# Optimization experiments

Measured on AMD Instinct MI355X. Metric: run time of the kernel, lower is better.

Reference implementation:

```python
import jax, jax.numpy as jnp
import numpy as np

N, E, D_IN, HD, H = 50000, 800000, 768, 64, 4
HC = HD * H


def _gat(x, src, dst, etypes, lin_w, att_src, att_dst, edge_emb, lin_edge_w, att_edge,
         bias, res_w, res_b, ln_g, ln_b):
    # Faithful PyG GATConv (edge_dim, concat=True, add_self_loops=True with
    # fill_value='mean', negative_slope=0.2) + residual + LayerNorm. Eval mode: no dropout.
    n = x.shape[0]
    h, c = att_src.shape
    xs = (x @ lin_w).reshape(n, h, c)                      # [N,H,C]
    a_src = jnp.einsum('nhc,hc->nh', xs, att_src)          # [N,H]
    a_dst = jnp.einsum('nhc,hc->nh', xs, att_dst)
    eattr = edge_emb[etypes]                               # [E,ed]
    ones = jnp.ones((etypes.shape[0],), x.dtype)
    cnt = jax.ops.segment_sum(ones, dst, num_segments=n)
    # self-loop edge_attr = mean of incoming edge attrs per node (fill_value='mean')
    loop_attr = jax.ops.segment_sum(eattr, dst, num_segments=n) / jnp.maximum(cnt, 1.0)[:, None]
    loop = jnp.arange(n, dtype=src.dtype)
    src_a = jnp.concatenate([src, loop])
    dst_a = jnp.concatenate([dst, loop])
    e_all = jnp.concatenate([eattr, loop_attr], 0)
    a_edge = jnp.einsum('ehc,hc->eh', (e_all @ lin_edge_w).reshape(-1, h, c), att_edge)
    alpha = jax.nn.leaky_relu(a_src[src_a] + a_dst[dst_a] + a_edge, 0.2)   # [Ea,H]
    # edge softmax over incoming edges of each destination node
    amax = jax.ops.segment_max(alpha, dst_a, num_segments=n)
    ea = jnp.exp(alpha - amax[dst_a])
    denom = jax.ops.segment_sum(ea, dst_a, num_segments=n)
    w = ea / (denom[dst_a] + 1e-16)
    out = jax.ops.segment_sum(xs[src_a] * w[:, :, None], dst_a, num_segments=n)
    out = out.reshape(n, h * c) + bias + (x @ res_w + res_b)
    mu = out.mean(-1, keepdims=True)
    var = jnp.mean((out - mu) ** 2, -1, keepdims=True)
    return (out - mu) * jax.lax.rsqrt(var + 1e-5) * ln_g + ln_b


def _forward(features, positions,
             fe_w1, fe_b1, fe_w2, fe_b2, fe_pos_w, fe_pos_b, fe_type_emb, fe_out_w, fe_out_b,
             g1_lin_w, g1_att_src, g1_att_dst, g1_edge_emb, g1_lin_edge_w, g1_att_edge,
             g1_bias, g1_res_w, g1_res_b, g1_ln_g, g1_ln_b,
             g2_lin_w, g2_att_src, g2_att_dst, g2_edge_emb, g2_lin_edge_w, g2_att_edge,
             g2_bias, g2_res_w, g2_res_b, g2_ln_g, g2_ln_b,
             cls_w, cls_b,
             edge_index, aspect_indices, edge_types, node_types):
    # EnhancedFeatureExtractor (eval: dropout = identity)
    hfe = jax.nn.relu(features @ fe_w1 + fe_b1) @ fe_w2 + fe_b2
    hfe = hfe + fe_type_emb[node_types] + positions[:, None] @ fe_pos_w + fe_pos_b
    hfe = hfe @ fe_out_w + fe_out_b
    src, dst = edge_index[0], edge_index[1]
    hid = _gat(hfe, src, dst, edge_types, g1_lin_w, g1_att_src, g1_att_dst, g1_edge_emb,
               g1_lin_edge_w, g1_att_edge, g1_bias, g1_res_w, g1_res_b, g1_ln_g, g1_ln_b)
    hid = jax.nn.relu(hid)
    hid = _gat(hid, src, dst, edge_types, g2_lin_w, g2_att_src, g2_att_dst, g2_edge_emb,
               g2_lin_edge_w, g2_att_edge, g2_bias, g2_res_w, g2_res_b, g2_ln_g, g2_ln_b)
    return hid[aspect_indices] @ cls_w + cls_b


def setup_inputs() -> dict:
    key = jax.random.key(0)
    ks = jax.random.split(key, 40)
    d = {}
    d['features'] = jax.random.normal(ks[0], (N, D_IN), jnp.float32)
    d['edge_index'] = jax.random.randint(ks[1], (2, E), 0, N, jnp.int32)
    d['aspect_indices'] = jax.random.randint(ks[2], (4096,), 0, N, jnp.int32)
    d['edge_types'] = jax.random.randint(ks[3], (E,), 0, 4, jnp.int32)
    d['node_types'] = jax.random.randint(ks[4], (N,), 0, 3, jnp.int32)
    d['positions'] = jax.random.uniform(ks[5], (N,), jnp.float32)

    def rn(i, shape, s=0.05):
        return s * jax.random.normal(ks[i], shape, jnp.float32)

    d['fe_w1'] = rn(6, (D_IN, HD)); d['fe_b1'] = rn(7, (HD,))
    d['fe_w2'] = rn(8, (HD, HD));   d['fe_b2'] = rn(9, (HD,))
    d['fe_pos_w'] = rn(10, (1, HD)); d['fe_pos_b'] = rn(11, (HD,))
    d['fe_type_emb'] = rn(12, (3, HD))
    d['fe_out_w'] = rn(13, (HD, HD)); d['fe_out_b'] = rn(14, (HD,))
    d['g1_lin_w'] = rn(15, (HD, HC))
    d['g1_att_src'] = rn(16, (H, HD)); d['g1_att_dst'] = rn(17, (H, HD))
    d['g1_edge_emb'] = rn(18, (4, 4)); d['g1_lin_edge_w'] = rn(19, (4, HC))
    d['g1_att_edge'] = rn(20, (H, HD))
    d['g1_bias'] = rn(21, (HC,)); d['g1_res_w'] = rn(22, (HD, HC)); d['g1_res_b'] = rn(23, (HC,))
    d['g1_ln_g'] = jnp.ones((HC,), jnp.float32); d['g1_ln_b'] = jnp.zeros((HC,), jnp.float32)
    d['g2_lin_w'] = rn(24, (HC, HD))
    d['g2_att_src'] = rn(25, (1, HD)); d['g2_att_dst'] = rn(26, (1, HD))
    d['g2_edge_emb'] = rn(27, (4, 4)); d['g2_lin_edge_w'] = rn(28, (4, HD))
    d['g2_att_edge'] = rn(29, (1, HD))
    d['g2_bias'] = rn(30, (HD,)); d['g2_res_w'] = rn(31, (HC, HD)); d['g2_res_b'] = rn(32, (HD,))
    d['g2_ln_g'] = jnp.ones((HD,), jnp.float32); d['g2_ln_b'] = jnp.zeros((HD,), jnp.float32)
    d['cls_w'] = rn(33, (HD, 3)); d['cls_b'] = rn(34, (3,))
    return d


def reference(features, edge_index, aspect_indices, edge_types, node_types, positions,
              fe_w1, fe_b1, fe_w2, fe_b2, fe_pos_w, fe_pos_b, fe_type_emb, fe_out_w, fe_out_b,
              g1_lin_w, g1_att_src, g1_att_dst, g1_edge_emb, g1_lin_edge_w, g1_att_edge,
              g1_bias, g1_res_w, g1_res_b, g1_ln_g, g1_ln_b,
              g2_lin_w, g2_att_src, g2_att_dst, g2_edge_emb, g2_lin_edge_w, g2_att_edge,
              g2_bias, g2_res_w, g2_res_b, g2_ln_g, g2_ln_b,
              cls_w, cls_b):
    return _forward(features, positions,
                    fe_w1, fe_b1, fe_w2, fe_b2, fe_pos_w, fe_pos_b, fe_type_emb, fe_out_w, fe_out_b,
                    g1_lin_w, g1_att_src, g1_att_dst, g1_edge_emb, g1_lin_edge_w, g1_att_edge,
                    g1_bias, g1_res_w, g1_res_b, g1_ln_g, g1_ln_b,
                    g2_lin_w, g2_att_src, g2_att_dst, g2_edge_emb, g2_lin_edge_w, g2_att_edge,
                    g2_bias, g2_res_w, g2_res_b, g2_ln_g, g2_ln_b,
                    cls_w, cls_b,
                    edge_index, aspect_indices, edge_types, node_types)
```

## Files before the change

### kernel.cpp

```cpp
#include <hip/hip_runtime.h>


#define LRELU(x) ((x) > 0.f ? (x) : 0.2f * (x))

typedef __attribute__((ext_vector_type(8))) short short8;
typedef __attribute__((ext_vector_type(4))) float floatx4;

__device__ __forceinline__ unsigned short f2bf(float x) {
    union { float f; unsigned int u; } v; v.f = x;
    unsigned int r = (v.u + 0x7FFFu + ((v.u >> 16) & 1u)) >> 16;
    return (unsigned short)r;
}
__device__ __forceinline__ unsigned int pkbf(float lo, float hi) {
    unsigned int a = __float_as_uint(lo) + 0x8000u;
    unsigned int b = __float_as_uint(hi) + 0x8000u;
    return __builtin_amdgcn_perm(b, a, 0x07060302u);
}
__device__ __forceinline__ float bflo(unsigned int u) {
    return __uint_as_float(u << 16);
}
__device__ __forceinline__ float bfhi(unsigned int u) {
    return __uint_as_float(u & 0xFFFF0000u);
}
__device__ __forceinline__ float bf1(unsigned short u) {
    return __uint_as_float(((unsigned int)u) << 16);
}

__global__ __launch_bounds__(64) void k_tables(
    const float* __restrict__ e_emb1, const float* __restrict__ lew1,
    const float* __restrict__ ae1,
    const float* __restrict__ e_emb2, const float* __restrict__ lew2,
    const float* __restrict__ ae2,
    float* __restrict__ aet1, float* __restrict__ aet2)
{
    __shared__ float M1[16];
    __shared__ float M2[4];
    int t = threadIdx.x;
    if (t < 16) {
        int d = t >> 2, h = t & 3;
        float s = 0.f;
        for (int c = 0; c < 64; ++c) s += lew1[d * 256 + h * 64 + c] * ae1[h * 64 + c];
        M1[d * 4 + h] = s;
    }
    if (t < 4) {
        float s = 0.f;
        for (int c = 0; c < 64; ++c) s += lew2[t * 64 + c] * ae2[c];
        M2[t] = s;
    }
    __syncthreads();
    if (t < 16) {
        int ty = t >> 2, h = t & 3;
        float s = 0.f;
        for (int d = 0; d < 4; ++d) s += e_emb1[ty * 4 + d] * M1[d * 4 + h];
        aet1[ty * 4 + h] = s;
    }
    if (t < 4) {
        float s = 0.f;
        for (int d = 0; d < 4; ++d) s += e_emb2[t * 4 + d] * M2[d];
        aet2[t] = s;
    }
}

__global__ __launch_bounds__(256) void k_bswz_fe1(
    const float* __restrict__ w1, unsigned short* __restrict__ out)
{
    for (int idx = blockIdx.x * 256 + threadIdx.x; idx < 768 * 64;
         idx += gridDim.x * 256) {
        int k = idx >> 6, col = idx & 63;
        int c = k >> 6, kl = k & 63, kg = kl >> 3, j = kl & 7;
        out[((c * 8 + kg) * 64 + col) * 8 + j] = f2bf(w1[k * 64 + col]);
    }
}

template<int K, int NH>
__global__ __launch_bounds__(256) void k_bswz2(
    const float* __restrict__ B1, const float* __restrict__ B2,
    unsigned short* __restrict__ out)
{
    const int NC = 2 * NH;
    for (int idx = blockIdx.x * 256 + threadIdx.x; idx < K * NC;
         idx += gridDim.x * 256) {
        int k = idx / NC, col = idx % NC;
        float v = (col < NH) ? B1[k * NH + col] : B2[k * NH + col - NH];
        int c = k >> 6, kl = k & 63, kg = kl >> 3, j = kl & 7;
        int ct = col >> 7, cl = col & 127;
        out[(((c * (NC / 128) + ct) * 8 + kg) * 128 + cl) * 8 + j] = f2bf(v);
    }
}

__global__ __launch_bounds__(256) void k_fe1(
    const float* __restrict__ feat, const unsigned short* __restrict__ bswz,
    const float* __restrict__ b1, float* __restrict__ t1, int N)
{
    __shared__ __align__(16) unsigned short A_lds[8 * 64 * 8];
    int t = threadIdx.x;
    int wv = t >> 6, lane = t & 63;
    int quad = lane >> 4, l16 = lane & 15;
    long n0 = (long)blockIdx.x * 64;

    floatx4 acc[4];
#pragma unroll
    for (int i = 0; i < 4; ++i) acc[i] = (floatx4){0.f, 0.f, 0.f, 0.f};

    int srow = t >> 2, sf4 = t & 3;
    long arow = n0 + srow;
    if (arow >= N) arow = N - 1;
    const float* fbase = feat + arow * 768 + sf4 * 16;
    int col = wv * 16 + l16;

    for (int kc = 0; kc < 768; kc += 64) {
        __syncthreads();
        float4 v0 = *(const float4*)(fbase + kc);
        float4 v1 = *(const float4*)(fbase + kc + 4);
        float4 v2 = *(const float4*)(fbase + kc + 8);
        float4 v3 = *(const float4*)(fbase + kc + 12);
        uint4 w0 = {pkbf(v0.x, v0.y), pkbf(v0.z, v0.w),
                    pkbf(v1.x, v1.y), pkbf(v1.z, v1.w)};
        uint4 w1p = {pkbf(v2.x, v2.y), pkbf(v2.z, v2.w),
                     pkbf(v3.x, v3.y), pkbf(v3.z, v3.w)};
        *(uint4*)&A_lds[((2 * sf4) * 64 + srow) * 8] = w0;
        *(uint4*)&A_lds[((2 * sf4 + 1) * 64 + srow) * 8] = w1p;
        __syncthreads();
        int ci = kc >> 6;
#pragma unroll
        for (int s = 0; s < 2; ++s) {
            int kg0 = s * 4 + quad;
            short8 bfrag = *(const short8*)&bswz[((ci * 8 + kg0) * 64 + col) * 8];
#pragma unroll
            for (int mt = 0; mt < 4; ++mt) {
                short8 afrag = *(const short8*)&A_lds[(kg0 * 64 + mt * 16 + l16) * 8];
                acc[mt] = __builtin_amdgcn_mfma_f32_16x16x32_bf16(
                    afrag, bfrag, acc[mt], 0, 0, 0);
            }
        }
    }
    float bb = b1[col];
#pragma unroll
    for (int mt = 0; mt < 4; ++mt) {
#pragma unroll
        for (int r = 0; r < 4; ++r) {
            long m = n0 + mt * 16 + quad * 4 + r;
            if (m < N) t1[m * 64 + col] = fmaxf(acc[mt][r] + bb, 0.f);
        }
    }
}

__global__ __launch_bounds__(256) void k_fe2(
    const float* __restrict__ t1, const float* __restrict__ w2,
    const float* __restrict__ b2, const int* __restrict__ ntypes,
    const float* __restrict__ temb, const float* __restrict__ pos,
    const float* __restrict__ posw, const float* __restrict__ posb,
    const float* __restrict__ outw, const float* __restrict__ outb,
    float* __restrict__ hfe)
{
    __shared__ float l1[256];
    __shared__ float l2[256];
    int t = threadIdx.x;
    long base = (long)blockIdx.x * 256;
    l1[t] = t1[base + t];
    __syncthreads();
    int r = t >> 6, c = t & 63;
    float acc = 0.f;
#pragma unroll 8
    for (int k = 0; k < 64; ++k) acc += l1[r * 64 + k] * w2[k * 64 + c];
    long n = (long)blockIdx.x * 4 + r;
    int nt = ntypes[n];
    acc += b2[c] + temb[nt * 64 + c] + pos[n] * posw[c] + posb[c];
    l2[r * 64 + c] = acc;
    __syncthreads();
    float acc2 = 0.f;
#pragma unroll 8
    for (int k = 0; k < 64; ++k) acc2 += l2[r * 64 + k] * outw[k * 64 + c];
    hfe[n * 64 + c] = acc2 + outb[c];
}

template<int K, int NH>
__global__ __launch_bounds__(256) void k_prep_gemm(
    const float* __restrict__ A, const unsigned short* __restrict__ bswz,
    const float* __restrict__ bias, const float* __restrict__ res_b,
    unsigned short* __restrict__ xsb, float* __restrict__ resp, int N)
{
    constexpr int CT = (2 * NH) / 128;
    __shared__ __align__(16) unsigned short A_lds[8 * 64 * 8];
    int t = threadIdx.x;
    int wv = t >> 6, lane = t & 63;
    int quad = lane >> 4, l16 = lane & 15;
    long n0 = (long)blockIdx.x * 64;
    int by = blockIdx.y;

    floatx4 acc[4][2];
#pragma unroll
    for (int i = 0; i < 4; ++i)
#pragma unroll
        for (int j = 0; j < 2; ++j) acc[i][j] = (floatx4){0.f, 0.f, 0.f, 0.f};

    int srow = t >> 2, sf4 = t & 3;
    long arow = n0 + srow;
    if (arow >= N) arow = N - 1;
    const float* abase = A + arow * (long)K + sf4 * 16;

    for (int kc = 0; kc < K; kc += 64) {
        __syncthreads();
        float4 v0 = *(const float4*)(abase + kc);
        float4 v1 = *(const float4*)(abase + kc + 4);
        float4 v2 = *(const float4*)(abase + kc + 8);
        float4 v3 = *(const float4*)(abase + kc + 12);
        uint4 w0 = {pkbf(v0.x, v0.y), pkbf(v0.z, v0.w),
                    pkbf(v1.x, v1.y), pkbf(v1.z, v1.w)};
        uint4 w1p = {pkbf(v2.x, v2.y), pkbf(v2.z, v2.w),
                     pkbf(v3.x, v3.y), pkbf(v3.z, v3.w)};
        *(uint4*)&A_lds[((2 * sf4) * 64 + srow) * 8] = w0;
        *(uint4*)&A_lds[((2 * sf4 + 1) * 64 + srow) * 8] = w1p;
        __syncthreads();
        int ci = kc >> 6;
#pragma unroll
        for (int s = 0; s < 2; ++s) {
            int kg0 = s * 4 + quad;
#pragma unroll
            for (int nt = 0; nt < 2; ++nt) {
                short8 bfrag = *(const short8*)&bswz[
                    (((ci * CT + by) * 8 + kg0) * 128 + wv * 32 + nt * 16 + l16) * 8];
#pragma unroll
                for (int mt = 0; mt < 4; ++mt) {
                    short8 afrag = *(const short8*)&A_lds[(kg0 * 64 + mt * 16 + l16) * 8];
                    acc[mt][nt] = __builtin_amdgcn_mfma_f32_16x16x32_bf16(
                        afrag, bfrag, acc[mt][nt], 0, 0, 0);
                }
            }
        }
    }
#pragma unroll
    for (int nt = 0; nt < 2; ++nt) {
        int gc = by * 128 + wv * 32 + nt * 16 + l16;
        bool isl = gc < NH;
        int oc = isl ? gc : gc - NH;
        float badd = isl ? 0.f : (bias[oc] + res_b[oc]);
#pragma unroll
        for (int mt = 0; mt < 4; ++mt) {
#pragma unroll
            for (int r = 0; r < 4; ++r) {
                long m = n0 + mt * 16 + quad * 4 + r;
                if (m < N) {
                    float val = acc[mt][nt][r];
                    if (isl) xsb[m * NH + oc] = f2bf(val);
                    else     resp[m * NH + oc] = val + badd;
                }
            }
        }
    }
}

template<int H>
__global__ __launch_bounds__(256) void k_att(
    const unsigned short* __restrict__ xsb, const float* __restrict__ att_s,
    const float* __restrict__ att_d, float* __restrict__ a_src,
    float* __restrict__ a_dst, int N)
{
    int t = threadIdx.x;
    int wv = t >> 6, lane = t & 63;
    long n = (long)blockIdx.x * 4 + wv;
    if (n >= N) return;
    if (H == 4) {
        ushort4 u = *(const ushort4*)&xsb[n * 256 + lane * 4];
        float4 as = *(const float4*)&att_s[lane * 4];
        float4 ad = *(const float4*)&att_d[lane * 4];
        float x0 = bf1(u.x), x1 = bf1(u.y), x2 = bf1(u.z), x3 = bf1(u.w);
        float p = x0 * as.x + x1 * as.y + x2 * as.z + x3 * as.w;
        float q = x0 * ad.x + x1 * ad.y + x2 * ad.z + x3 * ad.w;
#pragma unroll
        for (int k = 8; k; k >>= 1) {
            p += __shfl_xor(p, k, 64);
            q += __shfl_xor(q, k, 64);
        }
        if ((lane & 15) == 0) {
            a_src[n * 4 + (lane >> 4)] = p;
            a_dst[n * 4 + (lane >> 4)] = q;
        }
    } else {
        float x = bf1(xsb[n * 64 + lane]);
        float p = x * att_s[lane];
        float q = x * att_d[lane];
#pragma unroll
        for (int k = 32; k; k >>= 1) {
            p += __shfl_xor(p, k, 64);
            q += __shfl_xor(q, k, 64);
        }
        if (lane == 0) { a_src[n] = p; a_dst[n] = q; }
    }
}

__global__ __launch_bounds__(256) void k_count(
    const int* __restrict__ dst, const int* __restrict__ et,
    int* __restrict__ cnt_t, int E)
{
    int e = blockIdx.x * 256 + threadIdx.x;
    if (e < E) atomicAdd(&cnt_t[dst[e] * 4 + et[e]], 1);
}

__global__ __launch_bounds__(256) void k_scan1(
    const int* __restrict__ cnt_t, int* __restrict__ row_off,
    int* __restrict__ blk_sums, int N)
{
    __shared__ int s[256];
    int t = threadIdx.x;
    int i = blockIdx.x * 256 + t;
    int v = 0;
    if (i < N) v = cnt_t[4 * i] + cnt_t[4 * i + 1] + cnt_t[4 * i + 2] + cnt_t[4 * i + 3];
    s[t] = v;
    __syncthreads();
    for (int off = 1; off < 256; off <<= 1) {
        int x = 0;
        if (t >= off) x = s[t - off];
        __syncthreads();
        s[t] += x;
        __syncthreads();
    }
    if (i < N) row_off[i] = s[t] - v;
    if (t == 255) blk_sums[blockIdx.x] = s[255];
}

__global__ __launch_bounds__(256) void k_scan2(int* __restrict__ blk_sums, int nb)
{
    __shared__ int s[256];
    int t = threadIdx.x;
    int v = (t < nb) ? blk_sums[t] : 0;
    s[t] = v;
    __syncthreads();
    for (int off = 1; off < 256; off <<= 1) {
        int x = 0;
        if (t >= off) x = s[t - off];
        __syncthreads();
        s[t] += x;
        __syncthreads();
    }
    if (t < nb) blk_sums[t] = s[t] - v;
}

__global__ __launch_bounds__(256) void k_scan3(
    int* __restrict__ row_off, int* __restrict__ cursor,
    const int* __restrict__ blk_sums, int N, int E)
{
    int t = threadIdx.x;
    int i = blockIdx.x * 256 + t;
    if (i < N) {
        int o = row_off[i] + blk_sums[blockIdx.x];
        row_off[i] = o;
        cursor[i] = o;
    }
    if (i == 0) row_off[N] = E;
}

__global__ __launch_bounds__(256) void k_scatter(
    const int* __restrict__ src, const int* __restrict__ dst,
    const int* __restrict__ et, int* __restrict__ cursor,
    int* __restrict__ csr_pack, int E)
{
    int e = blockIdx.x * 256 + threadIdx.x;
    if (e < E) {
        int d = dst[e];
        int pos = atomicAdd(&cursor[d], 1);
        csr_pack[pos] = src[e] | (et[e] << 28);
    }
}

__global__ __launch_bounds__(128) void k_gat1(
    const unsigned short* __restrict__ xs1b, const float* __restrict__ a_src,
    const float* __restrict__ a_dst, const int* __restrict__ row_off,
    const int* __restrict__ csr_pack,
    const int* __restrict__ cnt_t, const float* __restrict__ aet1,
    const float* __restrict__ ln_g, const float* __restrict__ ln_b,
    float* io)
{
    __shared__ __align__(16) float4 ws[2][64];
    __shared__ float2 aetp[2][4];
    __shared__ float red[4];
    int n = blockIdx.x;
    int t = threadIdx.x;
    int w = t >> 6, c = t & 63;
    int h0 = 2 * w;
    if (t < 8) {
        int w2 = t >> 2, ty = t & 3;
        aetp[w2][ty] = make_float2(aet1[ty * 4 + 2 * w2], aet1[ty * 4 + 2 * w2 + 1]);
    }
    int off = row_off[n], deg = row_off[n + 1] - off;
    float2 a_d = *(const float2*)&a_dst[n * 4 + h0];
    __syncthreads();
    float ael0 = 0.f, ael1 = 0.f;
    int degc = 0;
#pragma unroll
    for (int ty = 0; ty < 4; ++ty) {
        int ct = cnt_t[n * 4 + ty];
        degc += ct;
        float2 ae = aetp[w][ty];
        ael0 += (float)ct * ae.x;
        ael1 += (float)ct * ae.y;
    }
    float inv = (degc > 0) ? 1.f / (float)degc : 1.f;
    float2 a_s_self = *(const float2*)&a_src[n * 4 + h0];
    float al0 = a_s_self.x + a_d.x + ael0 * inv;
    float al1 = a_s_self.y + a_d.y + ael1 * inv;
    al0 = LRELU(al0); al1 = LRELU(al1);
    float wself0 = expf(al0), wself1 = expf(al1);
    int col = w * 128 + 2 * c;
    unsigned int uself = *(const unsigned int*)&xs1b[(long)n * 256 + col];
    float wself_l = (c < 32) ? wself0 : wself1;
    float acc0 = wself_l * bflo(uself);
    float acc1 = wself_l * bfhi(uself);
    float dp0 = 0.f, dp1 = 0.f;
    const unsigned short* xcol = xs1b + col;
    for (int base = 0; base < deg; base += 64) {
        int cnt = min(64, deg - base);
        float w0 = 0.f, w1 = 0.f;
        int s = 0;
        if (c < cnt) {
            int pk = csr_pack[off + base + c];
            s = pk & 0x0FFFFFFF;
            int ty = ((unsigned)pk) >> 28;
            float2 as2 = *(const float2*)&a_src[s * 4 + h0];
            float2 ae = aetp[w][ty];
            float a0 = as2.x + a_d.x + ae.x;
            float a1 = as2.y + a_d.y + ae.y;
            a0 = LRELU(a0); a1 = LRELU(a1);
            w0 = expf(a0); w1 = expf(a1);
        }
        dp0 += w0; dp1 += w1;
        ws[w][c] = make_float4(w0, w1, __int_as_float(s), 0.f);
        int cr = (cnt + 7) & ~7;
        for (int i = 0; i < cr; i += 8) {
#pragma unroll
            for (int u = 0; u < 8; ++u) {
                float4 p = ws[w][i + u];
                unsigned int uu = *(const unsigned int*)&xcol[
                    (long)__float_as_int(p.z) * 256];
                float wl = (c < 32) ? p.x : p.y;
                acc0 += wl * bflo(uu);
                acc1 += wl * bfhi(uu);
            }
        }
    }
#pragma unroll
    for (int k = 32; k; k >>= 1) {
        dp0 += __shfl_xor(dp0, k, 64);
        dp1 += __shfl_xor(dp1, k, 64);
    }
    float dsum = ((c < 32) ? dp0 + wself0 : dp1 + wself1) + 1e-16f;
    float2 res = *(const float2*)&io[(long)n * 256 + col];
    float v0 = acc0 / dsum + res.x;
    float v1 = acc1 / dsum + res.y;
    float s1 = v0 + v1, s2 = v0 * v0 + v1 * v1;
#pragma unroll
    for (int k = 32; k; k >>= 1) {
        s1 += __shfl_xor(s1, k, 64);
        s2 += __shfl_xor(s2, k, 64);
    }
    if (c == 0) { red[w] = s1; red[2 + w] = s2; }
    __syncthreads();
    float mu = (red[0] + red[1]) * (1.f / 256.f);
    float var = (red[2] + red[3]) * (1.f / 256.f) - mu * mu;
    float rs = rsqrtf(var + 1e-5f);
    float2 g = *(const float2*)&ln_g[col];
    float2 bln = *(const float2*)&ln_b[col];
    float y0 = fmaxf((v0 - mu) * rs * g.x + bln.x, 0.f);
    float y1 = fmaxf((v1 - mu) * rs * g.y + bln.y, 0.f);
    *(float2*)&io[(long)n * 256 + col] = make_float2(y0, y1);
}

__global__ __launch_bounds__(64) void k_gat2(
    const unsigned short* __restrict__ xs2b, const float* __restrict__ a_src,
    const float* __restrict__ a_dst, const int* __restrict__ row_off,
    const int* __restrict__ csr_pack,
    const int* __restrict__ cnt_t, const float* __restrict__ aet2,
    const float* __restrict__ ln_g, const float* __restrict__ ln_b,
    float* io)
{
    __shared__ __align__(8) float2 ws[64];
    __shared__ float aetl[4];
    int n = blockIdx.x;
    int c = threadIdx.x;
    if (c < 4) aetl[c] = aet2[c];
    int off = row_off[n], deg = row_off[n + 1] - off;
    float a_d = a_dst[n];
    float ael = 0.f;
    int degc = 0;
#pragma unroll
    for (int ty = 0; ty < 4; ++ty) {
        int ct = cnt_t[n * 4 + ty];
        degc += ct;
        ael += (float)ct * aet2[ty];
    }
    ael *= (degc > 0 ? 1.f / (float)degc : 1.f);
    float al = a_src[n] + a_d + ael;
    al = LRELU(al);
    float wself = expf(al);
    float acc = wself * bf1(xs2b[(long)n * 64 + c]);
    float dp = 0.f;
    const unsigned short* xcol = xs2b + c;
    for (int base = 0; base < deg; base += 64) {
        int cnt = min(64, deg - base);
        float we = 0.f;
        int s = 0;
        if (c < cnt) {
            int pk = csr_pack[off + base + c];
            s = pk & 0x0FFFFFFF;
            int ty = ((unsigned)pk) >> 28;
            float a = a_src[s] + a_d + aetl[ty];
            a = LRELU(a);
            we = expf(a);
        }
        dp += we;
        ws[c] = make_float2(we, __int_as_float(s));
        int cr = (cnt + 7) & ~7;
        for (int i = 0; i < cr; i += 8) {
#pragma unroll
            for (int u = 0; u < 8; ++u) {
                float2 p = ws[i + u];
                acc += p.x * bf1(xcol[(long)__float_as_int(p.y) * 64]);
            }
        }
    }
#pragma unroll
    for (int k = 32; k; k >>= 1) dp += __shfl_xor(dp, k, 64);
    float dsum = dp + wself + 1e-16f;
    float v = acc / dsum + io[(long)n * 64 + c];
    float s1 = v, s2 = v * v;
#pragma unroll
    for (int k = 32; k; k >>= 1) {
        s1 += __shfl_xor(s1, k, 64);
        s2 += __shfl_xor(s2, k, 64);
    }
    float mu = s1 * (1.f / 64.f);
    float var = s2 * (1.f / 64.f) - mu * mu;
    io[(long)n * 64 + c] = (v - mu) * rsqrtf(var + 1e-5f) * ln_g[c] + ln_b[c];
}

__global__ __launch_bounds__(256) void k_cls(
    const float* __restrict__ hid2, const int* __restrict__ asp,
    const float* __restrict__ w, const float* __restrict__ b,
    float* __restrict__ out)
{
    int g = blockIdx.x * 256 + threadIdx.x;
    int i = g / 3, j = g - i * 3;
    int a = asp[i];
    float acc = b[j];
#pragma unroll 8
    for (int cc = 0; cc < 64; ++cc) acc += hid2[(long)a * 64 + cc] * w[cc * 3 + j];
    out[i * 3 + j] = acc;
}

extern "C" void kernel_launch(void* const* d_in, const int* in_sizes, int n_in,
                              void* d_out, int out_size, void* d_ws, size_t ws_size,
                              hipStream_t stream)
{
    const float* features    = (const float*)d_in[0];
    const int*   edge_index  = (const int*)d_in[1];
    const int*   aspect      = (const int*)d_in[2];
    const int*   etypes      = (const int*)d_in[3];
    const int*   ntypes      = (const int*)d_in[4];
    const float* pos         = (const float*)d_in[5];
    const float* fe_w1       = (const float*)d_in[6];
    const float* fe_b1       = (const float*)d_in[7];
    const float* fe_w2       = (const float*)d_in[8];
    const float* fe_b2       = (const float*)d_in[9];
    const float* fe_pos_w    = (const float*)d_in[10];
    const float* fe_pos_b    = (const float*)d_in[11];
    const float* fe_type_emb = (const float*)d_in[12];
    const float* fe_out_w    = (const float*)d_in[13];
    const float* fe_out_b    = (const float*)d_in[14];
    const float* g1_lin_w    = (const float*)d_in[15];
    const float* g1_att_src  = (const float*)d_in[16];
    const float* g1_att_dst  = (const float*)d_in[17];
    const float* g1_edge_emb = (const float*)d_in[18];
    const float* g1_lin_edge = (const float*)d_in[19];
    const float* g1_att_edge = (const float*)d_in[20];
    const float* g1_bias     = (const float*)d_in[21];
    const float* g1_res_w    = (const float*)d_in[22];
    const float* g1_res_b    = (const float*)d_in[23];
    const float* g1_ln_g     = (const float*)d_in[24];
    const float* g1_ln_b     = (const float*)d_in[25];
    const float* g2_lin_w    = (const float*)d_in[26];
    const float* g2_att_src  = (const float*)d_in[27];
    const float* g2_att_dst  = (const float*)d_in[28];
    const float* g2_edge_emb = (const float*)d_in[29];
    const float* g2_lin_edge = (const float*)d_in[30];
    const float* g2_att_edge = (const float*)d_in[31];
    const float* g2_bias     = (const float*)d_in[32];
    const float* g2_res_w    = (const float*)d_in[33];
    const float* g2_res_b    = (const float*)d_in[34];
    const float* g2_ln_g     = (const float*)d_in[35];
    const float* g2_ln_b     = (const float*)d_in[36];
    const float* cls_w       = (const float*)d_in[37];
    const float* cls_b       = (const float*)d_in[38];

    const int N = in_sizes[0] / 768;
    const int E = in_sizes[1] / 2;
    const int* src = edge_index;
    const int* dst = edge_index + E;

    char* wsb = (char*)d_ws;
    size_t off = 0;
    auto alloc = [&](size_t bytes) -> char* {
        char* p = wsb + off;
        off += (bytes + 255) & ~(size_t)255;
        return p;
    };
    float* t1      = (float*)alloc((size_t)N * 64 * 4);
    float* hfe     = (float*)alloc((size_t)N * 64 * 4);
    unsigned short* xs1b = (unsigned short*)alloc((size_t)N * 256 * 2);
    unsigned short* xs2b = (unsigned short*)alloc((size_t)N * 64 * 2);
    float* rp1     = (float*)alloc((size_t)N * 256 * 4);
    float* rp2     = (float*)alloc((size_t)N * 64 * 4);
    float* a_src1  = (float*)alloc((size_t)N * 4 * 4);
    float* a_dst1  = (float*)alloc((size_t)N * 4 * 4);
    float* a_src2  = (float*)alloc((size_t)N * 4);
    float* a_dst2  = (float*)alloc((size_t)N * 4);
    int*   cnt_t   = (int*)alloc((size_t)N * 4 * 4);
    int*   row_off = (int*)alloc((size_t)(N + 1) * 4);
    int*   cursor  = (int*)alloc((size_t)N * 4);
    int*   blk     = (int*)alloc(1024);
    int*   csr_pack= (int*)alloc((size_t)E * 4);
    float* aet1    = (float*)alloc(64);
    float* aet2    = (float*)alloc(64);
    unsigned short* bz_fe1 = (unsigned short*)alloc(768 * 64 * 2);
    unsigned short* bz_p1  = (unsigned short*)alloc(64 * 512 * 2);
    unsigned short* bz_p2  = (unsigned short*)alloc(256 * 128 * 2);

    hipMemsetAsync(cnt_t, 0, (size_t)N * 4 * 4, stream);

    int mb = (N + 63) / 64;
    int ab = (N + 3) / 4;

    k_tables<<<1, 64, 0, stream>>>(g1_edge_emb, g1_lin_edge, g1_att_edge,
                                   g2_edge_emb, g2_lin_edge, g2_att_edge, aet1, aet2);
    k_bswz_fe1<<<48, 256, 0, stream>>>(fe_w1, bz_fe1);
    k_bswz2<64, 256><<<32, 256, 0, stream>>>(g1_lin_w, g1_res_w, bz_p1);
    k_bswz2<256, 64><<<32, 256, 0, stream>>>(g2_lin_w, g2_res_w, bz_p2);
    k_fe1<<<mb, 256, 0, stream>>>(features, bz_fe1, fe_b1, t1, N);
    k_fe2<<<N / 4, 256, 0, stream>>>(t1, fe_w2, fe_b2, ntypes, fe_type_emb, pos,
                                     fe_pos_w, fe_pos_b, fe_out_w, fe_out_b, hfe);
    k_prep_gemm<64, 256><<<dim3(mb, 4), 256, 0, stream>>>(
        hfe, bz_p1, g1_bias, g1_res_b, xs1b, rp1, N);
    k_att<4><<<ab, 256, 0, stream>>>(xs1b, g1_att_src, g1_att_dst, a_src1, a_dst1, N);
    int eblk = (E + 255) / 256;
    int nb = (N + 255) / 256;
    k_count<<<eblk, 256, 0, stream>>>(dst, etypes, cnt_t, E);
    k_scan1<<<nb, 256, 0, stream>>>(cnt_t, row_off, blk, N);
    k_scan2<<<1, 256, 0, stream>>>(blk, nb);
    k_scan3<<<nb, 256, 0, stream>>>(row_off, cursor, blk, N, E);
    k_scatter<<<eblk, 256, 0, stream>>>(src, dst, etypes, cursor, csr_pack, E);
    k_gat1<<<N, 128, 0, stream>>>(xs1b, a_src1, a_dst1, row_off, csr_pack,
                                  cnt_t, aet1, g1_ln_g, g1_ln_b, rp1);
    k_prep_gemm<256, 64><<<dim3(mb, 1), 256, 0, stream>>>(
        rp1, bz_p2, g2_bias, g2_res_b, xs2b, rp2, N);
    k_att<1><<<ab, 256, 0, stream>>>(xs2b, g2_att_src, g2_att_dst, a_src2, a_dst2, N);
    k_gat2<<<N, 64, 0, stream>>>(xs2b, a_src2, a_dst2, row_off, csr_pack,
                                 cnt_t, aet2, g2_ln_g, g2_ln_b, rp2);
    k_cls<<<(out_size + 255) / 256, 256, 0, stream>>>(rp2, aspect, cls_w, cls_b,
                                                      (float*)d_out);
}
```

Before: 641.6 us.

## Register-prefetch GEMM A tiles and vectorize GAT neighbor gathers across lane groups

The two MFMA GEMM kernels now load the next K-chunk of A into registers while the current chunk is consumed, so global load latency overlaps with the MFMA work. The GAT aggregation kernels are restructured so that each lane gathers 8 (gat1) or 4 (gat2) bf16 features with one wide load, and four lane groups process different neighbors in parallel before a shuffle reduction. This replaces many narrow gathers with fewer wide ones. The cost is more registers, extra cross-lane reductions, and LayerNorm statistics that must be rescaled because each value is now replicated across four lane groups.

```diff
diff --git a/kernel.cpp b/kernel.cpp
--- a/kernel.cpp
+++ b/kernel.cpp
@@ -108,18 +108,25 @@
     const float* fbase = feat + arow * 768 + sf4 * 16;
     int col = wv * 16 + l16;
 
+    float4 v0 = *(const float4*)(fbase);
+    float4 v1 = *(const float4*)(fbase + 4);
+    float4 v2 = *(const float4*)(fbase + 8);
+    float4 v3 = *(const float4*)(fbase + 12);
+
     for (int kc = 0; kc < 768; kc += 64) {
-        __syncthreads();
-        float4 v0 = *(const float4*)(fbase + kc);
-        float4 v1 = *(const float4*)(fbase + kc + 4);
-        float4 v2 = *(const float4*)(fbase + kc + 8);
-        float4 v3 = *(const float4*)(fbase + kc + 12);
         uint4 w0 = {pkbf(v0.x, v0.y), pkbf(v0.z, v0.w),
                     pkbf(v1.x, v1.y), pkbf(v1.z, v1.w)};
         uint4 w1p = {pkbf(v2.x, v2.y), pkbf(v2.z, v2.w),
                      pkbf(v3.x, v3.y), pkbf(v3.z, v3.w)};
+        __syncthreads();
         *(uint4*)&A_lds[((2 * sf4) * 64 + srow) * 8] = w0;
         *(uint4*)&A_lds[((2 * sf4 + 1) * 64 + srow) * 8] = w1p;
+        if (kc + 64 < 768) {
+            v0 = *(const float4*)(fbase + kc + 64);
+            v1 = *(const float4*)(fbase + kc + 68);
+            v2 = *(const float4*)(fbase + kc + 72);
+            v3 = *(const float4*)(fbase + kc + 76);
+        }
         __syncthreads();
         int ci = kc >> 6;
 #pragma unroll
@@ -199,18 +206,25 @@
     if (arow >= N) arow = N - 1;
     const float* abase = A + arow * (long)K + sf4 * 16;
 
+    float4 v0 = *(const float4*)(abase);
+    float4 v1 = *(const float4*)(abase + 4);
+    float4 v2 = *(const float4*)(abase + 8);
+    float4 v3 = *(const float4*)(abase + 12);
+
     for (int kc = 0; kc < K; kc += 64) {
-        __syncthreads();
-        float4 v0 = *(const float4*)(abase + kc);
-        float4 v1 = *(const float4*)(abase + kc + 4);
-        float4 v2 = *(const float4*)(abase + kc + 8);
-        float4 v3 = *(const float4*)(abase + kc + 12);
         uint4 w0 = {pkbf(v0.x, v0.y), pkbf(v0.z, v0.w),
                     pkbf(v1.x, v1.y), pkbf(v1.z, v1.w)};
         uint4 w1p = {pkbf(v2.x, v2.y), pkbf(v2.z, v2.w),
                      pkbf(v3.x, v3.y), pkbf(v3.z, v3.w)};
+        __syncthreads();
         *(uint4*)&A_lds[((2 * sf4) * 64 + srow) * 8] = w0;
         *(uint4*)&A_lds[((2 * sf4 + 1) * 64 + srow) * 8] = w1p;
+        if (kc + 64 < K) {
+            v0 = *(const float4*)(abase + kc + 64);
+            v1 = *(const float4*)(abase + kc + 68);
+            v2 = *(const float4*)(abase + kc + 72);
+            v3 = *(const float4*)(abase + kc + 76);
+        }
         __syncthreads();
         int ci = kc >> 6;
 #pragma unroll
@@ -377,6 +391,7 @@
     int n = blockIdx.x;
     int t = threadIdx.x;
     int w = t >> 6, c = t & 63;
+    int lc = c & 15, g = c >> 4;
     int h0 = 2 * w;
     if (t < 8) {
         int w2 = t >> 2, ty = t & 3;
@@ -401,13 +416,14 @@
     float al1 = a_s_self.y + a_d.y + ael1 * inv;
     al0 = LRELU(al0); al1 = LRELU(al1);
     float wself0 = expf(al0), wself1 = expf(al1);
-    int col = w * 128 + 2 * c;
-    unsigned int uself = *(const unsigned int*)&xs1b[(long)n * 256 + col];
-    float wself_l = (c < 32) ? wself0 : wself1;
-    float acc0 = wself_l * bflo(uself);
-    float acc1 = wself_l * bfhi(uself);
+
+    int col0 = w * 128 + lc * 8;
+    const unsigned short* xrow = xs1b + col0;
+    float acc[8];
+#pragma unroll
+    for (int j = 0; j < 8; ++j) acc[j] = 0.f;
     float dp0 = 0.f, dp1 = 0.f;
-    const unsigned short* xcol = xs1b + col;
+
     for (int base = 0; base < deg; base += 64) {
         int cnt = min(64, deg - base);
         float w0 = 0.f, w1 = 0.f;
@@ -428,13 +444,14 @@
         int cr = (cnt + 7) & ~7;
         for (int i = 0; i < cr; i += 8) {
 #pragma unroll
-            for (int u = 0; u < 8; ++u) {
-                float4 p = ws[w][i + u];
-                unsigned int uu = *(const unsigned int*)&xcol[
-                    (long)__float_as_int(p.z) * 256];
-                float wl = (c < 32) ? p.x : p.y;
-                acc0 += wl * bflo(uu);
-                acc1 += wl * bfhi(uu);
+            for (int u = 0; u < 2; ++u) {
+                float4 p = ws[w][i + u * 4 + g];
+                float wl = (lc < 8) ? p.x : p.y;
+                uint4 q = *(const uint4*)&xrow[(long)__float_as_int(p.z) * 256];
+                acc[0] += wl * bflo(q.x); acc[1] += wl * bfhi(q.x);
+                acc[2] += wl * bflo(q.y); acc[3] += wl * bfhi(q.y);
+                acc[4] += wl * bflo(q.z); acc[5] += wl * bfhi(q.z);
+                acc[6] += wl * bflo(q.w); acc[7] += wl * bfhi(q.w);
             }
         }
     }
@@ -443,26 +460,56 @@
         dp0 += __shfl_xor(dp0, k, 64);
         dp1 += __shfl_xor(dp1, k, 64);
     }
-    float dsum = ((c < 32) ? dp0 + wself0 : dp1 + wself1) + 1e-16f;
-    float2 res = *(const float2*)&io[(long)n * 256 + col];
-    float v0 = acc0 / dsum + res.x;
-    float v1 = acc1 / dsum + res.y;
-    float s1 = v0 + v1, s2 = v0 * v0 + v1 * v1;
+#pragma unroll
+    for (int j = 0; j < 8; ++j) {
+        acc[j] += __shfl_xor(acc[j], 16, 64);
+        acc[j] += __shfl_xor(acc[j], 32, 64);
+    }
+    uint4 us = *(const uint4*)&xrow[(long)n * 256];
+    float wself_l = (lc < 8) ? wself0 : wself1;
+    acc[0] += wself_l * bflo(us.x); acc[1] += wself_l * bfhi(us.x);
+    acc[2] += wself_l * bflo(us.y); acc[3] += wself_l * bfhi(us.y);
+    acc[4] += wself_l * bflo(us.z); acc[5] += wself_l * bfhi(us.z);
+    acc[6] += wself_l * bflo(us.w); acc[7] += wself_l * bfhi(us.w);
+    float dsum = ((lc < 8) ? dp0 + wself0 : dp1 + wself1) + 1e-16f;
+    float rd = 1.f / dsum;
+    float4 r0 = *(const float4*)&io[(long)n * 256 + col0];
+    float4 r1 = *(const float4*)&io[(long)n * 256 + col0 + 4];
+    float v[8];
+    v[0] = acc[0] * rd + r0.x; v[1] = acc[1] * rd + r0.y;
+    v[2] = acc[2] * rd + r0.z; v[3] = acc[3] * rd + r0.w;
+    v[4] = acc[4] * rd + r1.x; v[5] = acc[5] * rd + r1.y;
+    v[6] = acc[6] * rd + r1.z; v[7] = acc[7] * rd + r1.w;
+    float s1 = 0.f, s2 = 0.f;
+#pragma unroll
+    for (int j = 0; j < 8; ++j) { s1 += v[j]; s2 += v[j] * v[j]; }
 #pragma unroll
     for (int k = 32; k; k >>= 1) {
         s1 += __shfl_xor(s1, k, 64);
         s2 += __shfl_xor(s2, k, 64);
     }
-    if (c == 0) { red[w] = s1; red[2 + w] = s2; }
+    if (c == 0) { red[w] = s1 * 0.25f; red[2 + w] = s2 * 0.25f; }
     __syncthreads();
     float mu = (red[0] + red[1]) * (1.f / 256.f);
     float var = (red[2] + red[3]) * (1.f / 256.f) - mu * mu;
     float rs = rsqrtf(var + 1e-5f);
-    float2 g = *(const float2*)&ln_g[col];
-    float2 bln = *(const float2*)&ln_b[col];
-    float y0 = fmaxf((v0 - mu) * rs * g.x + bln.x, 0.f);
-    float y1 = fmaxf((v1 - mu) * rs * g.y + bln.y, 0.f);
-    *(float2*)&io[(long)n * 256 + col] = make_float2(y0, y1);
+    float4 lg0 = *(const float4*)&ln_g[col0];
+    float4 lg1 = *(const float4*)&ln_g[col0 + 4];
+    float4 lb0 = *(const float4*)&ln_b[col0];
+    float4 lb1 = *(const float4*)&ln_b[col0 + 4];
+    if (g == 0) {
+        float4 y0, y1;
+        y0.x = fmaxf((v[0] - mu) * rs * lg0.x + lb0.x, 0.f);
+        y0.y = fmaxf((v[1] - mu) * rs * lg0.y + lb0.y, 0.f);
+        y0.z = fmaxf((v[2] - mu) * rs * lg0.z + lb0.z, 0.f);
+        y0.w = fmaxf((v[3] - mu) * rs * lg0.w + lb0.w, 0.f);
+        y1.x = fmaxf((v[4] - mu) * rs * lg1.x + lb1.x, 0.f);
+        y1.y = fmaxf((v[5] - mu) * rs * lg1.y + lb1.y, 0.f);
+        y1.z = fmaxf((v[6] - mu) * rs * lg1.z + lb1.z, 0.f);
+        y1.w = fmaxf((v[7] - mu) * rs * lg1.w + lb1.w, 0.f);
+        *(float4*)&io[(long)n * 256 + col0] = y0;
+        *(float4*)&io[(long)n * 256 + col0 + 4] = y1;
+    }
 }
 
 __global__ __launch_bounds__(64) void k_gat2(
@@ -477,6 +524,7 @@
     __shared__ float aetl[4];
     int n = blockIdx.x;
     int c = threadIdx.x;
+    int lc = c & 15, g = c >> 4;
     if (c < 4) aetl[c] = aet2[c];
     int off = row_off[n], deg = row_off[n + 1] - off;
     float a_d = a_dst[n];
@@ -492,9 +540,11 @@
     float al = a_src[n] + a_d + ael;
     al = LRELU(al);
     float wself = expf(al);
-    float acc = wself * bf1(xs2b[(long)n * 64 + c]);
+
+    int colb = lc * 4;
+    const unsigned short* xrow = xs2b + colb;
+    float acc[4] = {0.f, 0.f, 0.f, 0.f};
     float dp = 0.f;
-    const unsigned short* xcol = xs2b + c;
     for (int base = 0; base < deg; base += 64) {
         int cnt = min(64, deg - base);
         float we = 0.f;
@@ -512,25 +562,50 @@
         int cr = (cnt + 7) & ~7;
         for (int i = 0; i < cr; i += 8) {
 #pragma unroll
-            for (int u = 0; u < 8; ++u) {
-                float2 p = ws[i + u];
-                acc += p.x * bf1(xcol[(long)__float_as_int(p.y) * 64]);
+            for (int u = 0; u < 2; ++u) {
+                float2 p = ws[i + u * 4 + g];
+                uint2 q = *(const uint2*)&xrow[(long)__float_as_int(p.y) * 64];
+                acc[0] += p.x * bflo(q.x); acc[1] += p.x * bfhi(q.x);
+                acc[2] += p.x * bflo(q.y); acc[3] += p.x * bfhi(q.y);
             }
         }
     }
 #pragma unroll
     for (int k = 32; k; k >>= 1) dp += __shfl_xor(dp, k, 64);
+#pragma unroll
+    for (int j = 0; j < 4; ++j) {
+        acc[j] += __shfl_xor(acc[j], 16, 64);
+        acc[j] += __shfl_xor(acc[j], 32, 64);
+    }
+    uint2 us = *(const uint2*)&xrow[(long)n * 64];
+    acc[0] += wself * bflo(us.x); acc[1] += wself * bfhi(us.x);
+    acc[2] += wself * bflo(us.y); acc[3] += wself * bfhi(us.y);
     float dsum = dp + wself + 1e-16f;
-    float v = acc / dsum + io[(long)n * 64 + c];
-    float s1 = v, s2 = v * v;
+    float rd = 1.f / dsum;
+    float4 r = *(const float4*)&io[(long)n * 64 + colb];
+    float v[4];
+    v[0] = acc[0] * rd + r.x; v[1] = acc[1] * rd + r.y;
+    v[2] = acc[2] * rd + r.z; v[3] = acc[3] * rd + r.w;
+    float s1 = v[0] + v[1] + v[2] + v[3];
+    float s2 = v[0] * v[0] + v[1] * v[1] + v[2] * v[2] + v[3] * v[3];
 #pragma unroll
     for (int k = 32; k; k >>= 1) {
         s1 += __shfl_xor(s1, k, 64);
         s2 += __shfl_xor(s2, k, 64);
     }
-    float mu = s1 * (1.f / 64.f);
-    float var = s2 * (1.f / 64.f) - mu * mu;
-    io[(long)n * 64 + c] = (v - mu) * rsqrtf(var + 1e-5f) * ln_g[c] + ln_b[c];
+    float mu = s1 * (1.f / 256.f);
+    float var = s2 * (1.f / 256.f) - mu * mu;
+    float rs = rsqrtf(var + 1e-5f);
+    if (g == 0) {
+        float4 lg = *(const float4*)&ln_g[colb];
+        float4 lb = *(const float4*)&ln_b[colb];
+        float4 y;
+        y.x = (v[0] - mu) * rs * lg.x + lb.x;
+        y.y = (v[1] - mu) * rs * lg.y + lb.y;
+        y.z = (v[2] - mu) * rs * lg.z + lb.z;
+        y.w = (v[3] - mu) * rs * lg.w + lb.w;
+        *(float4*)&io[(long)n * 64 + colb] = y;
+    }
 }
 
 __global__ __launch_bounds__(256) void k_cls(
```

Result: no change. 636.0 us (-0.9%).
